# Kernel optimization log

Hardware: AMD Instinct MI355X
Metric: run time of the kernel (lower is better)

Reference implementation:

```python
import jax, jax.numpy as jnp
import numpy as np

BAG, SEQ, D = 8, 512, 768      # docs per bag, seq len, bert hidden (d_model)
NB = 4                          # bridge spans kept per doc (subsampling cap regime)
NPD = 2 + NB                    # nodes per doc: h, t, bridges
N = BAG * NPD                   # total entity nodes in the bag graph (48)
T = N * N                       # matrix cells fed to MatTransformer (2304)
H = 8
DK = D // H                     # head dim 96
DFF, L = 1024, 4                # MatTransformer ffn width / num_layers
NREL = 97                       # num_relations (DocRED)
EPS = 1e-5


def _ln(x, g, b):
    m = jnp.mean(x, axis=-1, keepdims=True)
    v = jnp.var(x, axis=-1, keepdims=True)
    return (x - m) * jax.lax.rsqrt(v + EPS) * g + b


def setup_inputs() -> dict:
    key = jax.random.key(0)
    ks = jax.random.split(key, 16)
    s = 0.02
    p = {}
    # stand-in for BERT last hidden states
    p['embedding'] = jax.random.normal(ks[0], (BAG, SEQ, D), jnp.float32)
    # entity spans per doc: [h, t, b1..bNB] x (start, end) inclusive, from get_htb markers
    starts = jax.random.randint(ks[1], (BAG, NPD), 0, SEQ - 9)
    lens = jax.random.randint(ks[2], (BAG, NPD), 1, 9)
    p['spans'] = jnp.stack([starts, starts + lens - 1], axis=-1).astype(jnp.int32)
    # pairwise relation encoders wu / wv / ln1
    p['Wu'] = jax.random.normal(ks[3], (D, D)) * s; p['bu'] = jnp.zeros((D,))
    p['Wv'] = jax.random.normal(ks[4], (D, D)) * s; p['bv'] = jnp.zeros((D,))
    p['Wl'] = jax.random.normal(ks[5], (D, D)) * s; p['bl'] = jnp.zeros((D,))
    # MatTransformer: L layers of MHA + FFN, params stacked over layers
    p['Wq'] = jax.random.normal(ks[6], (L, D, D)) * s;  p['bq'] = jnp.zeros((L, D))
    p['Wk'] = jax.random.normal(ks[7], (L, D, D)) * s;  p['bk'] = jnp.zeros((L, D))
    p['Wvm'] = jax.random.normal(ks[8], (L, D, D)) * s; p['bvm'] = jnp.zeros((L, D))
    p['Wo'] = jax.random.normal(ks[9], (L, D, D)) * s;  p['bo'] = jnp.zeros((L, D))
    p['F1'] = jax.random.normal(ks[10], (L, D, DFF)) * s; p['f1'] = jnp.zeros((L, DFF))
    p['F2'] = jax.random.normal(ks[11], (L, DFF, D)) * s; p['f2'] = jnp.zeros((L, D))
    p['g1'] = jnp.ones((L, D)); p['be1'] = jnp.zeros((L, D))
    p['g2'] = jnp.ones((L, D)); p['be2'] = jnp.zeros((L, D))
    # final norm + predictor
    p['ng'] = jnp.ones((D,)); p['nb'] = jnp.zeros((D,))
    p['Wp'] = jax.random.normal(ks[12], (D, NREL)) * s; p['bp'] = jnp.zeros((NREL,))
    return p


def _forward(embedding, spans, Wu, bu, Wv, bv, Wl, bl, Wq, bq, Wk, bk, Wvm, bvm,
             Wo, bo, F1, f1, F2, f2, g1, be1, g2, be2, ng, nb, Wp, bp):
    # --- ragged span gather + max pooling (masked max, vectorized) ---
    pos = jnp.arange(SEQ)
    m = (pos >= spans[..., :1]) & (pos <= spans[..., 1:])          # [BAG, NPD, SEQ]
    neg = jnp.finfo(embedding.dtype).min
    pooled = jnp.max(jnp.where(m[..., None], embedding[:, None, :, :], neg), axis=2)  # [BAG, NPD, D]
    htb = pooled.reshape(N, D)                                      # h/t/bridge node embs
    # --- pairwise outer-sum relation encoding: relu(ln1(relu(u_i + v_j))) ---
    u = htb @ Wu + bu
    v = htb @ Wv + bv
    rel = jax.nn.relu(jax.nn.relu(u[:, None, :] + v[None, :, :]) @ Wl + bl)  # [N, N, D]
    # --- MatTransformer: multi-head self-attention over the N*N matrix cells ---
    x = rel.reshape(T, D)
    scale = 1.0 / np.sqrt(DK).astype(np.float32)
    for l in range(L):
        q = (x @ Wq[l] + bq[l]).reshape(T, H, DK)
        k = (x @ Wk[l] + bk[l]).reshape(T, H, DK)
        vv = (x @ Wvm[l] + bvm[l]).reshape(T, H, DK)
        att = jax.nn.softmax(jnp.einsum('qhd,khd->hqk', q, k) * scale, axis=-1)
        o = jnp.einsum('hqk,khd->qhd', att, vv).reshape(T, D) @ Wo[l] + bo[l]
        x = _ln(x + o, g1[l], be1[l])
        f = jax.nn.relu(x @ F1[l] + f1[l]) @ F2[l] + f2[l]
        x = _ln(x + f, g2[l], be2[l])
    rel_m = x.reshape(N, N, D)
    # --- gather (h_pos, t_pos) cells: h at i*NPD, t at i*NPD+1 ---
    hp = jnp.arange(BAG) * NPD
    t_feature = rel_m[hp, hp + 1]                                   # [BAG, D]
    ht_logits = _ln(t_feature, ng, nb) @ Wp + bp                    # [BAG, NREL]
    bag_logit = jnp.max(ht_logits, axis=0, keepdims=True)           # [1, NREL]
    return bag_logit, ht_logits


def reference(embedding, spans, Wu, bu, Wv, bv, Wl, bl, Wq, bq, Wk, bk, Wvm, bvm,
              Wo, bo, F1, f1, F2, f2, g1, be1, g2, be2, ng, nb, Wp, bp):
    return _forward(embedding, spans, Wu, bu, Wv, bv, Wl, bl, Wq, bq, Wk, bk,
                    Wvm, bvm, Wo, bo, F1, f1, F2, f2, g1, be1, g2, be2, ng, nb, Wp, bp)
```

## Files before the change

kernel.cpp:

```cpp
#include <hip/hip_runtime.h>
#include <hip/hip_bf16.h>

typedef __hip_bfloat16 bf16;
typedef __bf16 bf16x8 __attribute__((ext_vector_type(8)));
typedef float f32x4 __attribute__((ext_vector_type(4)));

#define BAG 8
#define SEQ 512
#define DM 768
#define NPD 6
#define NNODE 48
#define TT 2304
#define NH 8
#define DKH 96
#define DFF 1024
#define NLAYER 4
#define NREL 97
#define SP 6
#define KSPAN (TT / SP)
#define LN_EPS 1e-5f

__device__ __forceinline__ float b2f(const bf16 x) { return __bfloat162float(x); }
__device__ __forceinline__ bf16 f2b(float f) { return __float2bfloat16(f); }
__device__ __forceinline__ unsigned short f2bu(float f) {
    bf16 h = __float2bfloat16(f);
    return *reinterpret_cast<unsigned short*>(&h);
}

__global__ __launch_bounds__(256) void span_pool(const float* __restrict__ emb,
                                                 const int* __restrict__ spans,
                                                 bf16* __restrict__ htb) {
    const int n = blockIdx.x;
    const int b = n / NPD;
    int s0 = spans[n * 2 + 0];
    int s1 = spans[n * 2 + 1];
    s0 = min(max(s0, 0), SEQ - 1);
    s1 = min(max(s1, s0), SEQ - 1);
    const float* base = emb + (size_t)b * SEQ * DM;
    for (int d = threadIdx.x; d < DM; d += 256) {
        float m = -3.0e38f;
        for (int s = s0; s <= s1; ++s) m = fmaxf(m, base[(size_t)s * DM + d]);
        htb[(size_t)n * DM + d] = f2b(m);
    }
}

__global__ __launch_bounds__(256) void prep_wt3(const float* __restrict__ W0,
                                                const float* __restrict__ W1,
                                                const float* __restrict__ W2,
                                                bf16* __restrict__ Wt) {
    __shared__ __align__(16) __bf16 tile[64][72];
    const int z = blockIdx.z;
    const float* W = (z == 0) ? W0 : (z == 1) ? W1 : W2;
    bf16* out = Wt + (size_t)z * DM * DM;
    const int t = threadIdx.x;
    const int k0 = blockIdx.x * 64, n0 = blockIdx.y * 64;
    const int r = t >> 2, cg = (t & 3) * 16;
#pragma unroll
    for (int i = 0; i < 4; ++i) {
        const float4 v = *(const float4*)&W[(size_t)(k0 + r) * DM + n0 + cg + 4 * i];
        tile[r][cg + 4 * i + 0] = (__bf16)v.x;
        tile[r][cg + 4 * i + 1] = (__bf16)v.y;
        tile[r][cg + 4 * i + 2] = (__bf16)v.z;
        tile[r][cg + 4 * i + 3] = (__bf16)v.w;
    }
    __syncthreads();
#pragma unroll
    for (int i = 0; i < 2; ++i) {
        bf16x8 o;
#pragma unroll
        for (int j = 0; j < 8; ++j) o[j] = tile[cg + 8 * i + j][r];
        *(bf16x8*)&out[(size_t)(n0 + r) * DM + k0 + cg + 8 * i] = o;
    }
}

__global__ __launch_bounds__(256) void prep6(const float* __restrict__ Wq,
                                             const float* __restrict__ Wk,
                                             const float* __restrict__ Wv,
                                             const float* __restrict__ Wo,
                                             const float* __restrict__ F1,
                                             const float* __restrict__ F2,
                                             bf16* __restrict__ slab) {
    __shared__ __align__(16) __bf16 tile[64][72];
    const int z = blockIdx.z;
    int K = DM, N = DM;
    const float* W;
    size_t off;
    switch (z) {
        case 0: W = Wq; off = 0;       break;
        case 1: W = Wk; off = 589824;  break;
        case 2: W = Wv; off = 1179648; break;
        case 3: W = Wo; off = 1769472; break;
        case 4: W = F1; off = 2359296; N = DFF; break;
        default: W = F2; off = 3145728; K = DFF; break;
    }
    const int k0 = blockIdx.x * 64, n0 = blockIdx.y * 64;
    if (k0 >= K || n0 >= N) return;
    bf16* out = slab + off;
    const int t = threadIdx.x;
    const int r = t >> 2, cg = (t & 3) * 16;
#pragma unroll
    for (int i = 0; i < 4; ++i) {
        const float4 v = *(const float4*)&W[(size_t)(k0 + r) * N + n0 + cg + 4 * i];
        tile[r][cg + 4 * i + 0] = (__bf16)v.x;
        tile[r][cg + 4 * i + 1] = (__bf16)v.y;
        tile[r][cg + 4 * i + 2] = (__bf16)v.z;
        tile[r][cg + 4 * i + 3] = (__bf16)v.w;
    }
    __syncthreads();
#pragma unroll
    for (int i = 0; i < 2; ++i) {
        bf16x8 o;
#pragma unroll
        for (int j = 0; j < 8; ++j) o[j] = tile[cg + 8 * i + j][r];
        *(bf16x8*)&out[(size_t)(n0 + r) * K + k0 + cg + 8 * i] = o;
    }
}

template <int RELU>
__global__ __launch_bounds__(128) void gemm_bt(const bf16* __restrict__ A,
                                               const bf16* __restrict__ Bt,
                                               const float* __restrict__ bias,
                                               bf16* __restrict__ C,
                                               int M, int N, int K) {
    __shared__ __align__(16) __bf16 As[2][32][72];
    __shared__ __align__(16) __bf16 Bs[2][64][72];
    const int t = threadIdx.x;
    const int w = t >> 6, lane = t & 63;
    const int quad = lane >> 4, l15 = lane & 15;
    const int row0 = blockIdx.y * 32, col0 = blockIdx.x * 64;
    const int a_row = t >> 2, a_oct = (t & 3) * 8;
    const int b_row = t >> 1, b_base = (t & 1) * 8;
    const bool a_ok = (row0 + a_row) < M;

    const f32x4 fz = {0.f, 0.f, 0.f, 0.f};
    f32x4 acc[4];
#pragma unroll
    for (int i = 0; i < 4; ++i) acc[i] = fz;

    bf16x8 av0, av1, bv[4];
    if (a_ok) {
        av0 = *(const bf16x8*)&A[(size_t)(row0 + a_row) * K + a_oct];
        av1 = *(const bf16x8*)&A[(size_t)(row0 + a_row) * K + 32 + a_oct];
    } else {
        for (int j = 0; j < 8; ++j) { av0[j] = (__bf16)0.0f; av1[j] = (__bf16)0.0f; }
    }
#pragma unroll
    for (int j = 0; j < 4; ++j)
        bv[j] = *(const bf16x8*)&Bt[(size_t)(col0 + b_row) * K + b_base + 16 * j];

    int cur = 0;
    for (int k0 = 0; k0 < K; k0 += 64) {
        *(bf16x8*)&As[cur][a_row][a_oct] = av0;
        *(bf16x8*)&As[cur][a_row][32 + a_oct] = av1;
#pragma unroll
        for (int j = 0; j < 4; ++j) *(bf16x8*)&Bs[cur][b_row][b_base + 16 * j] = bv[j];
        __syncthreads();

        if (k0 + 64 < K) {
            if (a_ok) {
                av0 = *(const bf16x8*)&A[(size_t)(row0 + a_row) * K + k0 + 64 + a_oct];
                av1 = *(const bf16x8*)&A[(size_t)(row0 + a_row) * K + k0 + 96 + a_oct];
            }
#pragma unroll
            for (int j = 0; j < 4; ++j)
                bv[j] = *(const bf16x8*)&Bt[(size_t)(col0 + b_row) * K + k0 + 64 + b_base + 16 * j];
        }

#pragma unroll
        for (int kk = 0; kk < 2; ++kk) {
            const bf16x8 af = *(const bf16x8*)&As[cur][16 * w + l15][quad * 8 + 32 * kk];
#pragma unroll
            for (int nt = 0; nt < 4; ++nt) {
                const bf16x8 bfv = *(const bf16x8*)&Bs[cur][16 * nt + l15][quad * 8 + 32 * kk];
                acc[nt] = __builtin_amdgcn_mfma_f32_16x16x32_bf16(af, bfv, acc[nt], 0, 0, 0);
            }
        }
        cur ^= 1;
    }

#pragma unroll
    for (int nt = 0; nt < 4; ++nt) {
        const int col = col0 + 16 * nt + l15;
        const float bvl = bias[col];
#pragma unroll
        for (int r = 0; r < 4; ++r) {
            const int row = row0 + 16 * w + quad * 4 + r;
            if (row < M) {
                float v = acc[nt][r] + bvl;
                if (RELU) v = fmaxf(v, 0.f);
                C[(size_t)row * N + col] = f2b(v);
            }
        }
    }
}

__global__ __launch_bounds__(128) void gemm_qkv(const bf16* __restrict__ A,
                                                const bf16* __restrict__ Bt,
                                                const float* __restrict__ b0,
                                                const float* __restrict__ b1,
                                                const float* __restrict__ b2,
                                                bf16* __restrict__ C0,
                                                bf16* __restrict__ C1,
                                                bf16* __restrict__ Vt) {
    __shared__ __align__(16) __bf16 As[32][72];
    __shared__ __align__(16) __bf16 Bs[64][72];
    const int t = threadIdx.x;
    const int w = t >> 6, lane = t & 63;
    const int quad = lane >> 4, l15 = lane & 15;
    const int row0 = blockIdx.y * 32, col0 = blockIdx.x * 64;
    const int a_row = t >> 2, a_oct = (t & 3) * 8;
    const int b_row = t >> 1, b_base = (t & 1) * 8;

    const f32x4 fz = {0.f, 0.f, 0.f, 0.f};
    f32x4 acc[4];
#pragma unroll
    for (int i = 0; i < 4; ++i) acc[i] = fz;

    bf16x8 av0, av1, bv[4];
    av0 = *(const bf16x8*)&A[(size_t)(row0 + a_row) * DM + a_oct];
    av1 = *(const bf16x8*)&A[(size_t)(row0 + a_row) * DM + 32 + a_oct];
#pragma unroll
    for (int j = 0; j < 4; ++j)
        bv[j] = *(const bf16x8*)&Bt[(size_t)(col0 + b_row) * DM + b_base + 16 * j];

    for (int k0 = 0; k0 < DM; k0 += 64) {
        *(bf16x8*)&As[a_row][a_oct] = av0;
        *(bf16x8*)&As[a_row][32 + a_oct] = av1;
#pragma unroll
        for (int j = 0; j < 4; ++j) *(bf16x8*)&Bs[b_row][b_base + 16 * j] = bv[j];
        __syncthreads();

        if (k0 + 64 < DM) {
            av0 = *(const bf16x8*)&A[(size_t)(row0 + a_row) * DM + k0 + 64 + a_oct];
            av1 = *(const bf16x8*)&A[(size_t)(row0 + a_row) * DM + k0 + 96 + a_oct];
#pragma unroll
            for (int j = 0; j < 4; ++j)
                bv[j] = *(const bf16x8*)&Bt[(size_t)(col0 + b_row) * DM + k0 + 64 + b_base + 16 * j];
        }

#pragma unroll
        for (int kk = 0; kk < 2; ++kk) {
            const bf16x8 af = *(const bf16x8*)&As[16 * w + l15][quad * 8 + 32 * kk];
#pragma unroll
            for (int nt = 0; nt < 4; ++nt) {
                const bf16x8 bfv = *(const bf16x8*)&Bs[16 * nt + l15][quad * 8 + 32 * kk];
                acc[nt] = __builtin_amdgcn_mfma_f32_16x16x32_bf16(af, bfv, acc[nt], 0, 0, 0);
            }
        }
        __syncthreads();
    }

    const int buf = col0 / DM;
    const int lc0 = col0 - buf * DM;
    if (buf < 2) {
        bf16* Cb = (buf == 0) ? C0 : C1;
        const float* bb = (buf == 0) ? b0 : b1;
#pragma unroll
        for (int nt = 0; nt < 4; ++nt) {
            const int col = lc0 + 16 * nt + l15;
            const float bvl = bb[col];
#pragma unroll
            for (int r = 0; r < 4; ++r) {
                const int row = row0 + 16 * w + quad * 4 + r;
                Cb[(size_t)row * DM + col] = f2b(acc[nt][r] + bvl);
            }
        }
    } else {
#pragma unroll
        for (int nt = 0; nt < 4; ++nt) {
            const float bvl = b2[lc0 + 16 * nt + l15];
#pragma unroll
            for (int r = 0; r < 4; ++r)
                Bs[16 * nt + l15][16 * w + quad * 4 + r] = (__bf16)(acc[nt][r] + bvl);
        }
        __syncthreads();
        const int c = t >> 1, half = (t & 1) * 16;
        const bf16x8 o0 = *(const bf16x8*)&Bs[c][half];
        const bf16x8 o1 = *(const bf16x8*)&Bs[c][half + 8];
        *(bf16x8*)&Vt[(size_t)(lc0 + c) * TT + row0 + half] = o0;
        *(bf16x8*)&Vt[(size_t)(lc0 + c) * TT + row0 + half + 8] = o1;
    }
}

template <int RELU>
__global__ __launch_bounds__(128) void gemm_mfma(const bf16* __restrict__ A,
                                                 const float* __restrict__ W,
                                                 const float* __restrict__ bias,
                                                 bf16* __restrict__ C,
                                                 int M, int N, int K) {
    __shared__ __align__(16) __bf16 As[32][40];
    __shared__ __align__(16) __bf16 Bs[64][40];
    const int t = threadIdx.x;
    const int w = t >> 6, lane = t & 63;
    const int quad = lane >> 4, l15 = lane & 15;
    const int row0 = blockIdx.y * 32, col0 = blockIdx.x * 64;
    const int s_row = t >> 2, s_kg = (t & 3) * 8;
    const int s_colg = (t & 15) * 4, s_kp = t >> 4;
    const bool a_ok = (row0 + s_row) < M;
    const f32x4 fz = {0.f, 0.f, 0.f, 0.f};
    f32x4 acc[4];
#pragma unroll
    for (int i = 0; i < 4; ++i) acc[i] = fz;

    for (int k0 = 0; k0 < K; k0 += 32) {
        bf16x8 av;
        for (int j = 0; j < 8; ++j) av[j] = (__bf16)0.0f;
        if (a_ok) av = *(const bf16x8*)&A[(size_t)(row0 + s_row) * K + k0 + s_kg];
        *(bf16x8*)&As[s_row][s_kg] = av;
#pragma unroll
        for (int rep = 0; rep < 2; ++rep) {
            const int kp = s_kp + 8 * rep;
            const size_t gb = (size_t)(k0 + 2 * kp) * N + col0 + s_colg;
            const float4 w0 = *(const float4*)&W[gb];
            const float4 w1 = *(const float4*)&W[gb + N];
#pragma unroll
            for (int i = 0; i < 4; ++i) {
                ushort2 pk;
                pk.x = f2bu((&w0.x)[i]);
                pk.y = f2bu((&w1.x)[i]);
                *(ushort2*)&Bs[s_colg + i][2 * kp] = pk;
            }
        }
        __syncthreads();
        const bf16x8 af = *(const bf16x8*)&As[16 * w + l15][quad * 8];
#pragma unroll
        for (int nt = 0; nt < 4; ++nt) {
            const bf16x8 bfv = *(const bf16x8*)&Bs[16 * nt + l15][quad * 8];
            acc[nt] = __builtin_amdgcn_mfma_f32_16x16x32_bf16(af, bfv, acc[nt], 0, 0, 0);
        }
        __syncthreads();
    }
#pragma unroll
    for (int nt = 0; nt < 4; ++nt) {
        const int col = col0 + 16 * nt + l15;
        const float bvl = bias[col];
#pragma unroll
        for (int r = 0; r < 4; ++r) {
            const int row = row0 + 16 * w + quad * 4 + r;
            if (row < M) {
                float v = acc[nt][r] + bvl;
                if (RELU) v = fmaxf(v, 0.f);
                C[(size_t)row * N + col] = f2b(v);
            }
        }
    }
}

__global__ __launch_bounds__(256) void build_relA(const bf16* __restrict__ u,
                                                  const bf16* __restrict__ v,
                                                  bf16* __restrict__ A) {
    const int cell = blockIdx.x;
    const int i = cell / NNODE, j = cell % NNODE;
    for (int k = threadIdx.x; k < DM; k += 256) {
        A[(size_t)cell * DM + k] = f2b(fmaxf(b2f(u[i * DM + k]) + b2f(v[j * DM + k]), 0.f));
    }
}

__global__ __launch_bounds__(256) void transpose_v(const bf16* __restrict__ v,
                                                   bf16* __restrict__ vt) {
    __shared__ __align__(16) __bf16 tile[64][72];
    const int t = threadIdx.x;
    const int bx = blockIdx.x, by = blockIdx.y;
    const int r = t >> 2, cg = (t & 3) * 16;
#pragma unroll
    for (int i = 0; i < 2; ++i)
        *(bf16x8*)&tile[r][cg + 8 * i] =
            *(const bf16x8*)&v[(size_t)(by * 64 + r) * DM + bx * 64 + cg + 8 * i];
    __syncthreads();
#pragma unroll
    for (int i = 0; i < 2; ++i) {
        bf16x8 o;
#pragma unroll
        for (int j = 0; j < 8; ++j) o[j] = tile[cg + 8 * i + j][r];
        *(bf16x8*)&vt[(size_t)(bx * 64 + r) * TT + by * 64 + cg + 8 * i] = o;
    }
}

template <int MODE>
__global__ __launch_bounds__(256) void attn_mfma(const bf16* __restrict__ qb,
                                                 const bf16* __restrict__ kb,
                                                 const bf16* __restrict__ vtb,
                                                 bf16* __restrict__ ob,
                                                 bf16* __restrict__ Opb,
                                                 float* __restrict__ Lp,
                                                 int kspan) {
    __shared__ __align__(16) __bf16 Ks[64][104];
    __shared__ __align__(16) __bf16 Vts[96][72];
    __shared__ __align__(16) __bf16 Ps[4][16][72];

    const int t = threadIdx.x;
    const int w = t >> 6, lane = t & 63;
    const int quad = lane >> 4, l15 = lane & 15;
    const int h = blockIdx.y;
    const int q0 = blockIdx.x * 64;
    const int p = blockIdx.z;
    const int kstart = p * kspan;
    const float scale = 0.10206207261596575f;

    bf16x8 qf[3];
#pragma unroll
    for (int ks = 0; ks < 3; ++ks) {
        qf[ks] = *(const bf16x8*)&qb[(size_t)(q0 + 16 * w + l15) * DM + h * DKH + quad * 8 + 32 * ks];
#pragma unroll
        for (int j = 0; j < 8; ++j) qf[ks][j] = (__bf16)((float)qf[ks][j] * scale);
    }

    const f32x4 fz = {0.f, 0.f, 0.f, 0.f};
    f32x4 Oa[6];
#pragma unroll
    for (int i = 0; i < 6; ++i) Oa[i] = fz;
    float lrow[4] = {0.f, 0.f, 0.f, 0.f};

    bf16x8 kreg[3], vreg[3];
#pragma unroll
    for (int i = 0; i < 3; ++i) {
        const int idx = t + 256 * i;
        const int r = idx / 12, c = idx % 12;
        kreg[i] = *(const bf16x8*)&kb[(size_t)(kstart + r) * DM + h * DKH + c * 8];
        const int d = idx >> 3, ck = idx & 7;
        vreg[i] = *(const bf16x8*)&vtb[(size_t)(h * DKH + d) * TT + kstart + ck * 8];
    }

    for (int kc = kstart; kc < kstart + kspan; kc += 64) {
        __syncthreads();
#pragma unroll
        for (int i = 0; i < 3; ++i) {
            const int idx = t + 256 * i;
            const int r = idx / 12, c = idx % 12;
            *(bf16x8*)&Ks[r][c * 8] = kreg[i];
            const int d = idx >> 3, ck = idx & 7;
            *(bf16x8*)&Vts[d][ck * 8] = vreg[i];
        }
        __syncthreads();

        if (kc + 64 < kstart + kspan) {
#pragma unroll
            for (int i = 0; i < 3; ++i) {
                const int idx = t + 256 * i;
                const int r = idx / 12, c = idx % 12;
                kreg[i] = *(const bf16x8*)&kb[(size_t)(kc + 64 + r) * DM + h * DKH + c * 8];
                const int d = idx >> 3, ck = idx & 7;
                vreg[i] = *(const bf16x8*)&vtb[(size_t)(h * DKH + d) * TT + kc + 64 + ck * 8];
            }
        }

        f32x4 Sa[4] = {fz, fz, fz, fz};
#pragma unroll
        for (int nt = 0; nt < 4; ++nt)
#pragma unroll
            for (int ks = 0; ks < 3; ++ks) {
                const bf16x8 kf = *(const bf16x8*)&Ks[l15 + 16 * nt][quad * 8 + 32 * ks];
                Sa[nt] = __builtin_amdgcn_mfma_f32_16x16x32_bf16(qf[ks], kf, Sa[nt], 0, 0, 0);
            }

#pragma unroll
        for (int r = 0; r < 4; ++r) {
            const float p0 = __expf(Sa[0][r]), p1 = __expf(Sa[1][r]);
            const float p2 = __expf(Sa[2][r]), p3 = __expf(Sa[3][r]);
            Ps[w][quad * 4 + r][l15]      = (__bf16)p0;
            Ps[w][quad * 4 + r][l15 + 16] = (__bf16)p1;
            Ps[w][quad * 4 + r][l15 + 32] = (__bf16)p2;
            Ps[w][quad * 4 + r][l15 + 48] = (__bf16)p3;
            float ps = p0 + p1 + p2 + p3;
            ps += __shfl_xor(ps, 1);
            ps += __shfl_xor(ps, 2);
            ps += __shfl_xor(ps, 4);
            ps += __shfl_xor(ps, 8);
            lrow[r] += ps;
        }

        const bf16x8 pa0 = *(const bf16x8*)&Ps[w][l15][quad * 8];
        const bf16x8 pa1 = *(const bf16x8*)&Ps[w][l15][32 + quad * 8];

#pragma unroll
        for (int nt = 0; nt < 6; ++nt) {
            const bf16x8 vf0 = *(const bf16x8*)&Vts[l15 + 16 * nt][quad * 8];
            const bf16x8 vf1 = *(const bf16x8*)&Vts[l15 + 16 * nt][32 + quad * 8];
            Oa[nt] = __builtin_amdgcn_mfma_f32_16x16x32_bf16(pa0, vf0, Oa[nt], 0, 0, 0);
            Oa[nt] = __builtin_amdgcn_mfma_f32_16x16x32_bf16(pa1, vf1, Oa[nt], 0, 0, 0);
        }
    }

    if (MODE == 0) {
#pragma unroll
        for (int nt = 0; nt < 6; ++nt)
#pragma unroll
            for (int r = 0; r < 4; ++r) {
                const int row = q0 + 16 * w + quad * 4 + r;
                ob[(size_t)row * DM + h * DKH + 16 * nt + l15] = f2b(Oa[nt][r] / lrow[r]);
            }
    } else {
#pragma unroll
        for (int nt = 0; nt < 6; ++nt)
#pragma unroll
            for (int r = 0; r < 4; ++r) {
                const int row = q0 + 16 * w + quad * 4 + r;
                Opb[((size_t)p * TT + row) * DM + h * DKH + 16 * nt + l15] = f2b(Oa[nt][r]);
            }
        if (l15 == 0) {
#pragma unroll
            for (int r = 0; r < 4; ++r) {
                const int row = q0 + 16 * w + quad * 4 + r;
                Lp[((size_t)p * NH + h) * TT + row] = lrow[r];
            }
        }
    }
}

__global__ __launch_bounds__(256) void attn_merge(const bf16* __restrict__ Opb,
                                                  const float* __restrict__ Lp,
                                                  bf16* __restrict__ ob) {
    __shared__ float Ls[NH];
    const int row = blockIdx.x, t = threadIdx.x;
    if (t < NH) {
        float L = 0.f;
#pragma unroll
        for (int p = 0; p < SP; ++p) L += Lp[((size_t)p * NH + t) * TT + row];
        Ls[t] = 1.0f / L;
    }
    __syncthreads();
#pragma unroll
    for (int i = 0; i < 3; ++i) {
        const int d = t + 256 * i;
        const int h = d / DKH;
        float o = 0.f;
#pragma unroll
        for (int p = 0; p < SP; ++p)
            o += b2f(Opb[((size_t)p * TT + row) * DM + d]);
        ob[(size_t)row * DM + d] = f2b(o * Ls[h]);
    }
}

__global__ __launch_bounds__(256) void add_ln(bf16* __restrict__ x,
                                              const bf16* __restrict__ r,
                                              const float* __restrict__ g,
                                              const float* __restrict__ be) {
    __shared__ float red[4];
    const int row = blockIdx.x;
    bf16* xr = x + (size_t)row * DM;
    const bf16* rr = r + (size_t)row * DM;
    const int t = threadIdx.x;

    float v0 = b2f(xr[t]) + b2f(rr[t]);
    float v1 = b2f(xr[t + 256]) + b2f(rr[t + 256]);
    float v2 = b2f(xr[t + 512]) + b2f(rr[t + 512]);
    float s = v0 + v1 + v2;
#pragma unroll
    for (int off = 32; off >= 1; off >>= 1) s += __shfl_xor(s, off);
    if ((t & 63) == 0) red[t >> 6] = s;
    __syncthreads();
    s = red[0] + red[1] + red[2] + red[3];
    const float mean = s * (1.f / 768.f);
    __syncthreads();

    const float d0 = v0 - mean, d1 = v1 - mean, d2 = v2 - mean;
    float ss = d0 * d0 + d1 * d1 + d2 * d2;
#pragma unroll
    for (int off = 32; off >= 1; off >>= 1) ss += __shfl_xor(ss, off);
    if ((t & 63) == 0) red[t >> 6] = ss;
    __syncthreads();
    ss = red[0] + red[1] + red[2] + red[3];
    const float inv = rsqrtf(ss * (1.f / 768.f) + LN_EPS);

    xr[t]       = f2b(d0 * inv * g[t]       + be[t]);
    xr[t + 256] = f2b(d1 * inv * g[t + 256] + be[t + 256]);
    xr[t + 512] = f2b(d2 * inv * g[t + 512] + be[t + 512]);
}

__global__ __launch_bounds__(256) void predict(const bf16* __restrict__ x,
                                               const float* __restrict__ ng,
                                               const float* __restrict__ nb,
                                               const float* __restrict__ Wp,
                                               const float* __restrict__ bp,
                                               float* __restrict__ out) {
    __shared__ float xs[BAG][DM];
    __shared__ float red[4][BAG];
    const int t = threadIdx.x;
    const int rel = blockIdx.x;
    const int wid = t >> 6, lane = t & 63;

    for (int rep = 0; rep < 2; ++rep) {
        const int b = wid + rep * 4;
        const bf16* row = x + (size_t)(294 * b + 1) * DM;
        float vals[12];
        float s = 0.f;
#pragma unroll
        for (int i = 0; i < 12; ++i) { vals[i] = b2f(row[lane + i * 64]); s += vals[i]; }
#pragma unroll
        for (int off = 32; off >= 1; off >>= 1) s += __shfl_xor(s, off);
        const float mean = s * (1.f / 768.f);
        float ss = 0.f;
#pragma unroll
        for (int i = 0; i < 12; ++i) { const float d = vals[i] - mean; ss += d * d; }
#pragma unroll
        for (int off = 32; off >= 1; off >>= 1) ss += __shfl_xor(ss, off);
        const float inv = rsqrtf(ss * (1.f / 768.f) + LN_EPS);
#pragma unroll
        for (int i = 0; i < 12; ++i) {
            const int d = lane + i * 64;
            xs[b][d] = (vals[i] - mean) * inv * ng[d] + nb[d];
        }
    }
    __syncthreads();

    float pb[BAG];
#pragma unroll
    for (int b = 0; b < BAG; ++b) pb[b] = 0.f;
    for (int k = t; k < DM; k += 256) {
        const float wv = Wp[(size_t)k * NREL + rel];
#pragma unroll
        for (int b = 0; b < BAG; ++b) pb[b] += xs[b][k] * wv;
    }
#pragma unroll
    for (int b = 0; b < BAG; ++b)
#pragma unroll
        for (int off = 32; off >= 1; off >>= 1) pb[b] += __shfl_xor(pb[b], off);
    if (lane == 0)
#pragma unroll
        for (int b = 0; b < BAG; ++b) red[wid][b] = pb[b];
    __syncthreads();
    if (t == 0) {
        float mx = -3.0e38f;
        for (int b = 0; b < BAG; ++b) {
            const float v = red[0][b] + red[1][b] + red[2][b] + red[3][b] + bp[rel];
            out[NREL + b * NREL + rel] = v;
            mx = fmaxf(mx, v);
        }
        out[rel] = mx;
    }
}

extern "C" void kernel_launch(void* const* d_in, const int* in_sizes, int n_in,
                              void* d_out, int out_size, void* d_ws, size_t ws_size,
                              hipStream_t stream) {
    const float* emb  = (const float*)d_in[0];
    const int* spans  = (const int*)d_in[1];
    const float* Wu = (const float*)d_in[2];  const float* bu = (const float*)d_in[3];
    const float* Wv = (const float*)d_in[4];  const float* bv = (const float*)d_in[5];
    const float* Wl = (const float*)d_in[6];  const float* bl = (const float*)d_in[7];
    const float* Wq = (const float*)d_in[8];  const float* bq = (const float*)d_in[9];
    const float* Wk = (const float*)d_in[10]; const float* bk = (const float*)d_in[11];
    const float* Wvm = (const float*)d_in[12]; const float* bvm = (const float*)d_in[13];
    const float* Wo = (const float*)d_in[14]; const float* bo = (const float*)d_in[15];
    const float* F1 = (const float*)d_in[16]; const float* f1 = (const float*)d_in[17];
    const float* F2 = (const float*)d_in[18]; const float* f2 = (const float*)d_in[19];
    const float* g1 = (const float*)d_in[20]; const float* be1 = (const float*)d_in[21];
    const float* g2 = (const float*)d_in[22]; const float* be2 = (const float*)d_in[23];
    const float* ng = (const float*)d_in[24]; const float* nb = (const float*)d_in[25];
    const float* Wp = (const float*)d_in[26]; const float* bp = (const float*)d_in[27];

    char* wsb = (char*)d_ws;
    bf16* htb = (bf16*)(wsb + 0);
    bf16* ub  = (bf16*)(wsb + 73728);
    bf16* vbn = (bf16*)(wsb + 147456);
    bf16* x   = (bf16*)(wsb + 221184);
    bf16* Bq  = (bf16*)(wsb + 3760128);
    bf16* Bk  = (bf16*)(wsb + 7299072);
    bf16* Bv  = (bf16*)(wsb + 10838016);
    bf16* Vt  = (bf16*)(wsb + 15556608);
    bf16* slab = (bf16*)(wsb + 19095552);
    bf16* Opb = (bf16*)(wsb + 26959872);
    float* Lp = (float*)(wsb + 48193536);

    const size_t FULL_END = 48635904;
    const bool use_full = ws_size >= FULL_END;

    span_pool<<<NNODE, 256, 0, stream>>>(emb, spans, htb);

    if (use_full) {
        prep_wt3<<<dim3(12, 12, 3), 256, 0, stream>>>(Wu, Wv, Wl, slab);
        gemm_bt<0><<<dim3(12, 2), 128, 0, stream>>>(htb, slab, bu, ub, NNODE, DM, DM);
        gemm_bt<0><<<dim3(12, 2), 128, 0, stream>>>(htb, slab + 589824, bv, vbn, NNODE, DM, DM);
        build_relA<<<TT, 256, 0, stream>>>(ub, vbn, Bq);
        gemm_bt<1><<<dim3(12, TT / 32), 128, 0, stream>>>(Bq, slab + 1179648, bl, x, TT, DM, DM);

        for (int l = 0; l < NLAYER; ++l) {
            const size_t wo = (size_t)l * DM * DM;
            const size_t f1o = (size_t)l * DM * DFF;
            prep6<<<dim3(16, 16, 6), 256, 0, stream>>>(Wq + wo, Wk + wo, Wvm + wo,
                                                       Wo + wo, F1 + f1o, F2 + f1o, slab);
            gemm_qkv<<<dim3(36, TT / 32), 128, 0, stream>>>(x, slab, bq + l * DM, bk + l * DM,
                                                            bvm + l * DM, Bq, Bk, Vt);
            attn_mfma<1><<<dim3(TT / 64, NH, SP), 256, 0, stream>>>(Bq, Bk, Vt, Bq, Opb, Lp, KSPAN);
            attn_merge<<<TT, 256, 0, stream>>>(Opb, Lp, Bq);
            gemm_bt<0><<<dim3(12, TT / 32), 128, 0, stream>>>(Bq, slab + 1769472, bo + l * DM, Bk, TT, DM, DM);
            add_ln<<<TT, 256, 0, stream>>>(x, Bk, g1 + l * DM, be1 + l * DM);
            gemm_bt<1><<<dim3(16, TT / 32), 128, 0, stream>>>(x, slab + 2359296, f1 + l * DFF, Bv, TT, DFF, DM);
            gemm_bt<0><<<dim3(12, TT / 32), 128, 0, stream>>>(Bv, slab + 3145728, f2 + l * DM, Bk, TT, DM, DFF);
            add_ln<<<TT, 256, 0, stream>>>(x, Bk, g2 + l * DM, be2 + l * DM);
        }
    } else {
        gemm_mfma<0><<<dim3(12, 2), 128, 0, stream>>>(htb, Wu, bu, ub, NNODE, DM, DM);
        gemm_mfma<0><<<dim3(12, 2), 128, 0, stream>>>(htb, Wv, bv, vbn, NNODE, DM, DM);
        build_relA<<<TT, 256, 0, stream>>>(ub, vbn, Bq);
        gemm_mfma<1><<<dim3(12, TT / 32), 128, 0, stream>>>(Bq, Wl, bl, x, TT, DM, DM);

        for (int l = 0; l < NLAYER; ++l) {
            const size_t wo = (size_t)l * DM * DM;
            const size_t f1o = (size_t)l * DM * DFF;
            gemm_mfma<0><<<dim3(12, TT / 32), 128, 0, stream>>>(x, Wq + wo, bq + l * DM, Bq, TT, DM, DM);
            gemm_mfma<0><<<dim3(12, TT / 32), 128, 0, stream>>>(x, Wk + wo, bk + l * DM, Bk, TT, DM, DM);
            gemm_mfma<0><<<dim3(12, TT / 32), 128, 0, stream>>>(x, Wvm + wo, bvm + l * DM, Bv, TT, DM, DM);
            transpose_v<<<dim3(DM / 64, TT / 64), 256, 0, stream>>>(Bv, Vt);
            attn_mfma<0><<<dim3(TT / 64, NH, 1), 256, 0, stream>>>(Bq, Bk, Vt, Bq, Opb, Lp, TT);
            gemm_mfma<0><<<dim3(12, TT / 32), 128, 0, stream>>>(Bq, Wo + wo, bo + l * DM, Bk, TT, DM, DM);
            add_ln<<<TT, 256, 0, stream>>>(x, Bk, g1 + l * DM, be1 + l * DM);
            gemm_mfma<1><<<dim3(16, TT / 32), 128, 0, stream>>>(x, F1 + f1o, f1 + l * DFF, Bv, TT, DFF, DM);
            gemm_mfma<0><<<dim3(12, TT / 32), 128, 0, stream>>>(Bv, F2 + f1o, f2 + l * DM, Bk, TT, DM, DFF);
            add_ln<<<TT, 256, 0, stream>>>(x, Bk, g2 + l * DM, be2 + l * DM);
        }
    }

    predict<<<NREL, 256, 0, stream>>>(x, ng, nb, Wp, bp, (float*)d_out);
}
```

Before: 713.3 us.

## Use 64x64 GEMM tiles, double-buffer QKV, vectorize attention merge, halve split-K

GEMM kernels now compute 64x64 output tiles per block, with each wave owning two 16-row MFMA strips. This doubles reuse of every B fragment and halves the block count. The fused QKV GEMM gains double-buffered shared memory, which removes its second barrier per k-step. The attention merge now processes 8 rows per block with 16-byte vector loads, and the attention key split count drops from 6 to 3, cutting the partial-result traffic at the cost of less parallelism in attention.

```diff
diff --git a/kernel.cpp b/kernel.cpp
--- a/kernel.cpp
+++ b/kernel.cpp
@@ -16,7 +16,7 @@
 #define DFF 1024
 #define NLAYER 4
 #define NREL 97
-#define SP 6
+#define SP 3
 #define KSPAN (TT / SP)
 #define LN_EPS 1e-5f
 
@@ -117,62 +117,68 @@
 }
 
 template <int RELU>
-__global__ __launch_bounds__(128) void gemm_bt(const bf16* __restrict__ A,
-                                               const bf16* __restrict__ Bt,
-                                               const float* __restrict__ bias,
-                                               bf16* __restrict__ C,
-                                               int M, int N, int K) {
-    __shared__ __align__(16) __bf16 As[2][32][72];
+__global__ __launch_bounds__(128) void gemm_bt64(const bf16* __restrict__ A,
+                                                 const bf16* __restrict__ Bt,
+                                                 const float* __restrict__ bias,
+                                                 bf16* __restrict__ C,
+                                                 int M, int N, int K) {
+    __shared__ __align__(16) __bf16 As[2][64][72];
     __shared__ __align__(16) __bf16 Bs[2][64][72];
     const int t = threadIdx.x;
     const int w = t >> 6, lane = t & 63;
     const int quad = lane >> 4, l15 = lane & 15;
-    const int row0 = blockIdx.y * 32, col0 = blockIdx.x * 64;
-    const int a_row = t >> 2, a_oct = (t & 3) * 8;
-    const int b_row = t >> 1, b_base = (t & 1) * 8;
-    const bool a_ok = (row0 + a_row) < M;
+    const int row0 = blockIdx.y * 64, col0 = blockIdx.x * 64;
+    const int s_row = t >> 1, s_off = (t & 1) * 32;
+    const bool a_ok = (row0 + s_row) < M;
 
     const f32x4 fz = {0.f, 0.f, 0.f, 0.f};
-    f32x4 acc[4];
-#pragma unroll
-    for (int i = 0; i < 4; ++i) acc[i] = fz;
-
-    bf16x8 av0, av1, bv[4];
-    if (a_ok) {
-        av0 = *(const bf16x8*)&A[(size_t)(row0 + a_row) * K + a_oct];
-        av1 = *(const bf16x8*)&A[(size_t)(row0 + a_row) * K + 32 + a_oct];
-    } else {
-        for (int j = 0; j < 8; ++j) { av0[j] = (__bf16)0.0f; av1[j] = (__bf16)0.0f; }
-    }
+    f32x4 acc[2][4];
+#pragma unroll
+    for (int m = 0; m < 2; ++m)
+#pragma unroll
+        for (int i = 0; i < 4; ++i) acc[m][i] = fz;
+
+    bf16x8 av[4], bv[4];
 #pragma unroll
     for (int j = 0; j < 4; ++j)
-        bv[j] = *(const bf16x8*)&Bt[(size_t)(col0 + b_row) * K + b_base + 16 * j];
+#pragma unroll
+        for (int e = 0; e < 8; ++e) av[j][e] = (__bf16)0.0f;
+    if (a_ok)
+#pragma unroll
+        for (int j = 0; j < 4; ++j)
+            av[j] = *(const bf16x8*)&A[(size_t)(row0 + s_row) * K + s_off + 8 * j];
+#pragma unroll
+    for (int j = 0; j < 4; ++j)
+        bv[j] = *(const bf16x8*)&Bt[(size_t)(col0 + s_row) * K + s_off + 8 * j];
 
     int cur = 0;
     for (int k0 = 0; k0 < K; k0 += 64) {
-        *(bf16x8*)&As[cur][a_row][a_oct] = av0;
-        *(bf16x8*)&As[cur][a_row][32 + a_oct] = av1;
-#pragma unroll
-        for (int j = 0; j < 4; ++j) *(bf16x8*)&Bs[cur][b_row][b_base + 16 * j] = bv[j];
+#pragma unroll
+        for (int j = 0; j < 4; ++j) {
+            *(bf16x8*)&As[cur][s_row][s_off + 8 * j] = av[j];
+            *(bf16x8*)&Bs[cur][s_row][s_off + 8 * j] = bv[j];
+        }
         __syncthreads();
 
         if (k0 + 64 < K) {
-            if (a_ok) {
-                av0 = *(const bf16x8*)&A[(size_t)(row0 + a_row) * K + k0 + 64 + a_oct];
-                av1 = *(const bf16x8*)&A[(size_t)(row0 + a_row) * K + k0 + 96 + a_oct];
-            }
+            if (a_ok)
+#pragma unroll
+                for (int j = 0; j < 4; ++j)
+                    av[j] = *(const bf16x8*)&A[(size_t)(row0 + s_row) * K + k0 + 64 + s_off + 8 * j];
 #pragma unroll
             for (int j = 0; j < 4; ++j)
-                bv[j] = *(const bf16x8*)&Bt[(size_t)(col0 + b_row) * K + k0 + 64 + b_base + 16 * j];
+                bv[j] = *(const bf16x8*)&Bt[(size_t)(col0 + s_row) * K + k0 + 64 + s_off + 8 * j];
         }
 
 #pragma unroll
         for (int kk = 0; kk < 2; ++kk) {
-            const bf16x8 af = *(const bf16x8*)&As[cur][16 * w + l15][quad * 8 + 32 * kk];
+            const bf16x8 af0 = *(const bf16x8*)&As[cur][32 * w + l15][quad * 8 + 32 * kk];
+            const bf16x8 af1 = *(const bf16x8*)&As[cur][32 * w + 16 + l15][quad * 8 + 32 * kk];
 #pragma unroll
             for (int nt = 0; nt < 4; ++nt) {
                 const bf16x8 bfv = *(const bf16x8*)&Bs[cur][16 * nt + l15][quad * 8 + 32 * kk];
-                acc[nt] = __builtin_amdgcn_mfma_f32_16x16x32_bf16(af, bfv, acc[nt], 0, 0, 0);
+                acc[0][nt] = __builtin_amdgcn_mfma_f32_16x16x32_bf16(af0, bfv, acc[0][nt], 0, 0, 0);
+                acc[1][nt] = __builtin_amdgcn_mfma_f32_16x16x32_bf16(af1, bfv, acc[1][nt], 0, 0, 0);
             }
         }
         cur ^= 1;
@@ -183,71 +189,78 @@
         const int col = col0 + 16 * nt + l15;
         const float bvl = bias[col];
 #pragma unroll
-        for (int r = 0; r < 4; ++r) {
-            const int row = row0 + 16 * w + quad * 4 + r;
-            if (row < M) {
-                float v = acc[nt][r] + bvl;
-                if (RELU) v = fmaxf(v, 0.f);
-                C[(size_t)row * N + col] = f2b(v);
-            }
-        }
-    }
-}
-
-__global__ __launch_bounds__(128) void gemm_qkv(const bf16* __restrict__ A,
-                                                const bf16* __restrict__ Bt,
-                                                const float* __restrict__ b0,
-                                                const float* __restrict__ b1,
-                                                const float* __restrict__ b2,
-                                                bf16* __restrict__ C0,
-                                                bf16* __restrict__ C1,
-                                                bf16* __restrict__ Vt) {
-    __shared__ __align__(16) __bf16 As[32][72];
-    __shared__ __align__(16) __bf16 Bs[64][72];
+        for (int m = 0; m < 2; ++m)
+#pragma unroll
+            for (int r = 0; r < 4; ++r) {
+                const int row = row0 + 32 * w + 16 * m + quad * 4 + r;
+                if (row < M) {
+                    float v = acc[m][nt][r] + bvl;
+                    if (RELU) v = fmaxf(v, 0.f);
+                    C[(size_t)row * N + col] = f2b(v);
+                }
+            }
+    }
+}
+
+__global__ __launch_bounds__(128) void gemm_qkv2(const bf16* __restrict__ A,
+                                                 const bf16* __restrict__ Bt,
+                                                 const float* __restrict__ b0,
+                                                 const float* __restrict__ b1,
+                                                 const float* __restrict__ b2,
+                                                 bf16* __restrict__ C0,
+                                                 bf16* __restrict__ C1,
+                                                 bf16* __restrict__ Vt) {
+    __shared__ __align__(16) __bf16 As[2][64][72];
+    __shared__ __align__(16) __bf16 Bs[2][64][72];
     const int t = threadIdx.x;
     const int w = t >> 6, lane = t & 63;
     const int quad = lane >> 4, l15 = lane & 15;
-    const int row0 = blockIdx.y * 32, col0 = blockIdx.x * 64;
-    const int a_row = t >> 2, a_oct = (t & 3) * 8;
-    const int b_row = t >> 1, b_base = (t & 1) * 8;
+    const int row0 = blockIdx.y * 64, col0 = blockIdx.x * 64;
+    const int s_row = t >> 1, s_off = (t & 1) * 32;
 
     const f32x4 fz = {0.f, 0.f, 0.f, 0.f};
-    f32x4 acc[4];
-#pragma unroll
-    for (int i = 0; i < 4; ++i) acc[i] = fz;
-
-    bf16x8 av0, av1, bv[4];
-    av0 = *(const bf16x8*)&A[(size_t)(row0 + a_row) * DM + a_oct];
-    av1 = *(const bf16x8*)&A[(size_t)(row0 + a_row) * DM + 32 + a_oct];
-#pragma unroll
-    for (int j = 0; j < 4; ++j)
-        bv[j] = *(const bf16x8*)&Bt[(size_t)(col0 + b_row) * DM + b_base + 16 * j];
-
+    f32x4 acc[2][4];
+#pragma unroll
+    for (int m = 0; m < 2; ++m)
+#pragma unroll
+        for (int i = 0; i < 4; ++i) acc[m][i] = fz;
+
+    bf16x8 av[4], bv[4];
+#pragma unroll
+    for (int j = 0; j < 4; ++j) {
+        av[j] = *(const bf16x8*)&A[(size_t)(row0 + s_row) * DM + s_off + 8 * j];
+        bv[j] = *(const bf16x8*)&Bt[(size_t)(col0 + s_row) * DM + s_off + 8 * j];
+    }
+
+    int cur = 0;
     for (int k0 = 0; k0 < DM; k0 += 64) {
-        *(bf16x8*)&As[a_row][a_oct] = av0;
-        *(bf16x8*)&As[a_row][32 + a_oct] = av1;
-#pragma unroll
-        for (int j = 0; j < 4; ++j) *(bf16x8*)&Bs[b_row][b_base + 16 * j] = bv[j];
+#pragma unroll
+        for (int j = 0; j < 4; ++j) {
+            *(bf16x8*)&As[cur][s_row][s_off + 8 * j] = av[j];
+            *(bf16x8*)&Bs[cur][s_row][s_off + 8 * j] = bv[j];
+        }
         __syncthreads();
 
         if (k0 + 64 < DM) {
-            av0 = *(const bf16x8*)&A[(size_t)(row0 + a_row) * DM + k0 + 64 + a_oct];
-            av1 = *(const bf16x8*)&A[(size_t)(row0 + a_row) * DM + k0 + 96 + a_oct];
-#pragma unroll
-            for (int j = 0; j < 4; ++j)
-                bv[j] = *(const bf16x8*)&Bt[(size_t)(col0 + b_row) * DM + k0 + 64 + b_base + 16 * j];
+#pragma unroll
+            for (int j = 0; j < 4; ++j) {
+                av[j] = *(const bf16x8*)&A[(size_t)(row0 + s_row) * DM + k0 + 64 + s_off + 8 * j];
+                bv[j] = *(const bf16x8*)&Bt[(size_t)(col0 + s_row) * DM + k0 + 64 + s_off + 8 * j];
+            }
         }
 
 #pragma unroll
         for (int kk = 0; kk < 2; ++kk) {
-            const bf16x8 af = *(const bf16x8*)&As[16 * w + l15][quad * 8 + 32 * kk];
+            const bf16x8 af0 = *(const bf16x8*)&As[cur][32 * w + l15][quad * 8 + 32 * kk];
+            const bf16x8 af1 = *(const bf16x8*)&As[cur][32 * w + 16 + l15][quad * 8 + 32 * kk];
 #pragma unroll
             for (int nt = 0; nt < 4; ++nt) {
-                const bf16x8 bfv = *(const bf16x8*)&Bs[16 * nt + l15][quad * 8 + 32 * kk];
-                acc[nt] = __builtin_amdgcn_mfma_f32_16x16x32_bf16(af, bfv, acc[nt], 0, 0, 0);
-            }
-        }
-        __syncthreads();
+                const bf16x8 bfv = *(const bf16x8*)&Bs[cur][16 * nt + l15][quad * 8 + 32 * kk];
+                acc[0][nt] = __builtin_amdgcn_mfma_f32_16x16x32_bf16(af0, bfv, acc[0][nt], 0, 0, 0);
+                acc[1][nt] = __builtin_amdgcn_mfma_f32_16x16x32_bf16(af1, bfv, acc[1][nt], 0, 0, 0);
+            }
+        }
+        cur ^= 1;
     }
 
     const int buf = col0 / DM;
@@ -260,25 +273,31 @@
             const int col = lc0 + 16 * nt + l15;
             const float bvl = bb[col];
 #pragma unroll
-            for (int r = 0; r < 4; ++r) {
-                const int row = row0 + 16 * w + quad * 4 + r;
-                Cb[(size_t)row * DM + col] = f2b(acc[nt][r] + bvl);
-            }
+            for (int m = 0; m < 2; ++m)
+#pragma unroll
+                for (int r = 0; r < 4; ++r) {
+                    const int row = row0 + 32 * w + 16 * m + quad * 4 + r;
+                    Cb[(size_t)row * DM + col] = f2b(acc[m][nt][r] + bvl);
+                }
         }
     } else {
+        __bf16 (*Tb)[72] = As[0];
+        __syncthreads();
 #pragma unroll
         for (int nt = 0; nt < 4; ++nt) {
             const float bvl = b2[lc0 + 16 * nt + l15];
 #pragma unroll
-            for (int r = 0; r < 4; ++r)
-                Bs[16 * nt + l15][16 * w + quad * 4 + r] = (__bf16)(acc[nt][r] + bvl);
+            for (int m = 0; m < 2; ++m)
+#pragma unroll
+                for (int r = 0; r < 4; ++r)
+                    Tb[16 * nt + l15][32 * w + 16 * m + quad * 4 + r] = (__bf16)(acc[m][nt][r] + bvl);
         }
         __syncthreads();
-        const int c = t >> 1, half = (t & 1) * 16;
-        const bf16x8 o0 = *(const bf16x8*)&Bs[c][half];
-        const bf16x8 o1 = *(const bf16x8*)&Bs[c][half + 8];
-        *(bf16x8*)&Vt[(size_t)(lc0 + c) * TT + row0 + half] = o0;
-        *(bf16x8*)&Vt[(size_t)(lc0 + c) * TT + row0 + half + 8] = o1;
+        const int c = t >> 1, half = (t & 1) * 32;
+#pragma unroll
+        for (int j = 0; j < 4; ++j)
+            *(bf16x8*)&Vt[(size_t)(lc0 + c) * TT + row0 + half + 8 * j] =
+                *(const bf16x8*)&Tb[c][half + 8 * j];
     }
 }
 
@@ -510,24 +529,36 @@
 __global__ __launch_bounds__(256) void attn_merge(const bf16* __restrict__ Opb,
                                                   const float* __restrict__ Lp,
                                                   bf16* __restrict__ ob) {
-    __shared__ float Ls[NH];
-    const int row = blockIdx.x, t = threadIdx.x;
-    if (t < NH) {
+    __shared__ float Ls[8][NH];
+    const int r0 = blockIdx.x * 8;
+    const int t = threadIdx.x;
+    if (t < 8 * NH) {
+        const int rl = t >> 3, hh = t & 7;
         float L = 0.f;
 #pragma unroll
-        for (int p = 0; p < SP; ++p) L += Lp[((size_t)p * NH + t) * TT + row];
-        Ls[t] = 1.0f / L;
-    }
-    __syncthreads();
-#pragma unroll
-    for (int i = 0; i < 3; ++i) {
-        const int d = t + 256 * i;
-        const int h = d / DKH;
-        float o = 0.f;
-#pragma unroll
-        for (int p = 0; p < SP; ++p)
-            o += b2f(Opb[((size_t)p * TT + row) * DM + d]);
-        ob[(size_t)row * DM + d] = f2b(o * Ls[h]);
+        for (int p = 0; p < SP; ++p) L += Lp[((size_t)p * NH + hh) * TT + r0 + rl];
+        Ls[rl][hh] = 1.0f / L;
+    }
+    __syncthreads();
+    const int rl = t >> 5, lane = t & 31;
+    const int row = r0 + rl;
+#pragma unroll
+    for (int j = 0; j < 3; ++j) {
+        const int d0 = lane * 8 + j * 256;
+        float acc[8];
+#pragma unroll
+        for (int e = 0; e < 8; ++e) acc[e] = 0.f;
+#pragma unroll
+        for (int p = 0; p < SP; ++p) {
+            const bf16x8 vv = *(const bf16x8*)&Opb[((size_t)p * TT + row) * DM + d0];
+#pragma unroll
+            for (int e = 0; e < 8; ++e) acc[e] += (float)vv[e];
+        }
+        const float s = Ls[rl][d0 / DKH];
+        bf16x8 o;
+#pragma unroll
+        for (int e = 0; e < 8; ++e) o[e] = (__bf16)(acc[e] * s);
+        *(bf16x8*)&ob[(size_t)row * DM + d0] = o;
     }
 }
 
@@ -669,24 +700,24 @@
 
     if (use_full) {
         prep_wt3<<<dim3(12, 12, 3), 256, 0, stream>>>(Wu, Wv, Wl, slab);
-        gemm_bt<0><<<dim3(12, 2), 128, 0, stream>>>(htb, slab, bu, ub, NNODE, DM, DM);
-        gemm_bt<0><<<dim3(12, 2), 128, 0, stream>>>(htb, slab + 589824, bv, vbn, NNODE, DM, DM);
+        gemm_bt64<0><<<dim3(12, 1), 128, 0, stream>>>(htb, slab, bu, ub, NNODE, DM, DM);
+        gemm_bt64<0><<<dim3(12, 1), 128, 0, stream>>>(htb, slab + 589824, bv, vbn, NNODE, DM, DM);
         build_relA<<<TT, 256, 0, stream>>>(ub, vbn, Bq);
-        gemm_bt<1><<<dim3(12, TT / 32), 128, 0, stream>>>(Bq, slab + 1179648, bl, x, TT, DM, DM);
+        gemm_bt64<1><<<dim3(12, TT / 64), 128, 0, stream>>>(Bq, slab + 1179648, bl, x, TT, DM, DM);
 
         for (int l = 0; l < NLAYER; ++l) {
             const size_t wo = (size_t)l * DM * DM;
             const size_t f1o = (size_t)l * DM * DFF;
             prep6<<<dim3(16, 16, 6), 256, 0, stream>>>(Wq + wo, Wk + wo, Wvm + wo,
                                                        Wo + wo, F1 + f1o, F2 + f1o, slab);
-            gemm_qkv<<<dim3(36, TT / 32), 128, 0, stream>>>(x, slab, bq + l * DM, bk + l * DM,
-                                                            bvm + l * DM, Bq, Bk, Vt);
+            gemm_qkv2<<<dim3(36, TT / 64), 128, 0, stream>>>(x, slab, bq + l * DM, bk + l * DM,
+                                                             bvm + l * DM, Bq, Bk, Vt);
             attn_mfma<1><<<dim3(TT / 64, NH, SP), 256, 0, stream>>>(Bq, Bk, Vt, Bq, Opb, Lp, KSPAN);
-            attn_merge<<<TT, 256, 0, stream>>>(Opb, Lp, Bq);
-            gemm_bt<0><<<dim3(12, TT / 32), 128, 0, stream>>>(Bq, slab + 1769472, bo + l * DM, Bk, TT, DM, DM);
+            attn_merge<<<TT / 8, 256, 0, stream>>>(Opb, Lp, Bq);
+            gemm_bt64<0><<<dim3(12, TT / 64), 128, 0, stream>>>(Bq, slab + 1769472, bo + l * DM, Bk, TT, DM, DM);
             add_ln<<<TT, 256, 0, stream>>>(x, Bk, g1 + l * DM, be1 + l * DM);
-            gemm_bt<1><<<dim3(16, TT / 32), 128, 0, stream>>>(x, slab + 2359296, f1 + l * DFF, Bv, TT, DFF, DM);
-            gemm_bt<0><<<dim3(12, TT / 32), 128, 0, stream>>>(Bv, slab + 3145728, f2 + l * DM, Bk, TT, DM, DFF);
+            gemm_bt64<1><<<dim3(16, TT / 64), 128, 0, stream>>>(x, slab + 2359296, f1 + l * DFF, Bv, TT, DFF, DM);
+            gemm_bt64<0><<<dim3(12, TT / 64), 128, 0, stream>>>(Bv, slab + 3145728, f2 + l * DM, Bk, TT, DM, DFF);
             add_ln<<<TT, 256, 0, stream>>>(x, Bk, g2 + l * DM, be2 + l * DM);
         }
     } else {
```

Result: slower. 749.2 us (+5.0%).
